# Optimization experiments

Measured on AMD Instinct MI355X. Metric: run time of the kernel, lower is better.

## Reference

```python
import jax, jax.numpy as jnp
import numpy as np

B, L, H, V = 32768, 24, 64, 64
EPS_NORM = 1e-12  # F.normalize eps
EPS_LN = 1e-5     # LayerNorm eps


def setup_inputs() -> dict:
    key = jax.random.key(0)
    ks = jax.random.split(key, 12)
    s = 1.0 / np.sqrt(H)
    init_val = float(np.log(0.9184 / (1.0 - 0.9184)))
    return {
        "seq": jax.random.randint(ks[0], (B, L), 0, V, dtype=jnp.int32),
        "embed": jax.random.normal(ks[1], (V, H), jnp.float32),
        "w1": jax.random.normal(ks[2], (H, 2 * H), jnp.float32) * s,
        "b1": jnp.zeros((2 * H,), jnp.float32),
        "w2": jax.random.normal(ks[3], (2 * H, H), jnp.float32) * s,
        "b2": jnp.zeros((H,), jnp.float32),
        "ln_g": jnp.ones((H,), jnp.float32),
        "ln_b": jnp.zeros((H,), jnp.float32),
        "rp_w": jax.random.normal(ks[4], (H, H), jnp.float32) * s,
        "rp_b": jnp.zeros((H,), jnp.float32),
        "out_w": jax.random.normal(ks[5], (H, V), jnp.float32) * s,
        "out_b": jnp.zeros((V,), jnp.float32),
        "alpha_logits": jnp.full((L,), init_val, jnp.float32),
    }


def _layernorm(x, g, b):
    mu = jnp.mean(x, axis=-1, keepdims=True)
    var = jnp.mean(jnp.square(x - mu), axis=-1, keepdims=True)
    return (x - mu) * jax.lax.rsqrt(var + EPS_LN) * g + b


def reference(seq, embed, w1, b1, w2, b2, ln_g, ln_b, rp_w, rp_b, out_w, out_b, alpha_logits):
    h = embed[seq]  # [B, L, H]
    ff = jax.nn.relu(h @ w1 + b1) @ w2 + b2
    h = _layernorm(h + ff, ln_g, ln_b)

    alphas = jax.nn.sigmoid(alpha_logits) * 0.49 + 0.5  # [L]
    ht = jnp.swapaxes(h[:, :-1, :], 0, 1)  # [L-1, B, H] time-major

    def step(M, inp):
        k, a = inp  # k: [B, H], a: scalar
        kn = k / jnp.maximum(jnp.linalg.norm(k, axis=-1, keepdims=True), EPS_NORM)
        vp = jnp.einsum('bij,bj->bi', M, kn)
        dv = k - vp
        M = M + (1.0 - a) * (dv[:, :, None] * kn[:, None, :])
        return M, None

    M0 = jnp.zeros((seq.shape[0], h.shape[-1], h.shape[-1]), h.dtype)
    M, _ = jax.lax.scan(step, M0, (ht, alphas[:-1]))

    v = jnp.einsum('bij,bj->bi', M, h[:, -1, :])
    return (v @ rp_w + rp_b) @ out_w + out_b  # [B, V]
```

## Files before the change

### kernel.cpp

```cpp
#include <hip/hip_runtime.h>
#include <hip/hip_bf16.h>
#include <math.h>

#define B_SZ 32768
#define L_SZ 24
#define H_SZ 64
#define V_SZ 64
#define ROW 68

#define HT_OFF 0
#define WK_OFF 4352
#define RN_OFF 8704
#define B2_OFF 8768
#define CF_OFF 8832
#define WS_FLOATS 8864

__global__ __launch_bounds__(128) void k_tables(
    const float* __restrict__ embed, const float* __restrict__ w1, const float* __restrict__ b1,
    const float* __restrict__ w2, const float* __restrict__ b2,
    const float* __restrict__ ln_g, const float* __restrict__ ln_b,
    float* __restrict__ ws)
{
  const int v = blockIdx.x;
  const int tid = threadIdx.x;
  __shared__ float e[H_SZ], hid[2 * H_SZ], x[H_SZ];

  if (tid < H_SZ) e[tid] = embed[v * H_SZ + tid];
  __syncthreads();

  float hj = b1[tid];
  #pragma unroll
  for (int h = 0; h < H_SZ; ++h) hj += e[h] * w1[h * (2 * H_SZ) + tid];
  hid[tid] = fmaxf(hj, 0.0f);
  __syncthreads();

  if (tid < H_SZ) {
    float f = b2[tid];
    #pragma unroll
    for (int j = 0; j < 2 * H_SZ; ++j) f += hid[j] * w2[j * H_SZ + tid];
    x[tid] = e[tid] + f;
  }
  __syncthreads();

  if (tid < H_SZ) {
    const float xi = x[tid];
    float mu = xi;
    #pragma unroll
    for (int m = 1; m < 64; m <<= 1) mu += __shfl_xor(mu, m);
    mu *= (1.0f / 64.0f);
    const float dv = xi - mu;
    float var = dv * dv;
    #pragma unroll
    for (int m = 1; m < 64; m <<= 1) var += __shfl_xor(var, m);
    var *= (1.0f / 64.0f);
    const float y = dv * rsqrtf(var + 1e-5f) * ln_g[tid] + ln_b[tid];
    ws[HT_OFF + v * ROW + tid] = y;
    float n2 = y * y;
    #pragma unroll
    for (int m = 1; m < 64; m <<= 1) n2 += __shfl_xor(n2, m);
    if (tid == 0) ws[RN_OFF + v] = 1.0f / fmaxf(sqrtf(n2), 1e-12f);
  }
}

__global__ __launch_bounds__(64) void k_proj(
    const float* __restrict__ rp_w, const float* __restrict__ rp_b,
    const float* __restrict__ out_w, const float* __restrict__ out_b,
    const float* __restrict__ alpha_logits, float* __restrict__ ws)
{
  const int i = blockIdx.x;
  const int j = threadIdx.x;
  if (i < V_SZ) {
    __shared__ float t1[H_SZ];
    float s = 0.0f;
    #pragma unroll
    for (int k = 0; k < H_SZ; ++k) s += ws[HT_OFF + i * ROW + k] * rp_w[k * H_SZ + j];
    t1[j] = s;
    __syncthreads();
    float s2 = 0.0f;
    #pragma unroll
    for (int k = 0; k < H_SZ; ++k) s2 += t1[k] * out_w[k * V_SZ + j];
    ws[WK_OFF + i * ROW + j] = s2;
  } else {
    float s = out_b[j];
    #pragma unroll
    for (int k = 0; k < H_SZ; ++k) s += rp_b[k] * out_w[k * V_SZ + j];
    ws[B2_OFF + j] = s;
    if (j < L_SZ - 1) {
      const float a = 1.0f / (1.0f + expf(-alpha_logits[j])) * 0.49f + 0.5f;
      ws[CF_OFF + j] = 1.0f - a;
    }
  }
}

__global__ __launch_bounds__(256) void k_scan(
    const int* __restrict__ seq, const float* __restrict__ ws, float* __restrict__ out)
{
  __shared__ float lds[WS_FLOATS];
  const int tid = threadIdx.x;
  for (int i = tid; i < WS_FLOATS / 4; i += 256)
    ((float4*)lds)[i] = ((const float4*)ws)[i];
  __syncthreads();

  const int lane = tid & 63;
  const int wv = tid >> 6;
  const int g = lane >> 2;
  const int s = lane & 3;
  const int batch = blockIdx.x * 64 + wv * 16 + g;
  const int s16 = s * 16;

  int sqv[L_SZ];
  const int4* sp = (const int4*)(seq + batch * L_SZ);
  #pragma unroll
  for (int i = 0; i < 6; ++i) ((int4*)sqv)[i] = sp[i];

  const float* hT = lds + HT_OFF;
  const float* wkT = lds + WK_OFF;
  const float* rnT = lds + RN_OFF;
  const float* b2T = lds + B2_OFF;
  const float* cfT = lds + CF_OFF;

  float qh[16], oa[16];
  {
    const float* qr = hT + sqv[L_SZ - 1] * ROW + s16;
    #pragma unroll
    for (int i = 0; i < 4; ++i) {
      const float4 q4 = *(const float4*)(qr + 4 * i);
      qh[4 * i + 0] = q4.x; qh[4 * i + 1] = q4.y; qh[4 * i + 2] = q4.z; qh[4 * i + 3] = q4.w;
    }
  }
  #pragma unroll
  for (int i = 0; i < 16; ++i) oa[i] = 0.0f;

  #pragma unroll
  for (int t = L_SZ - 2; t >= 0; --t) {
    const int tok = sqv[t];
    const float* kr = hT + tok * ROW + s16;
    float kv[16];
    #pragma unroll
    for (int i = 0; i < 4; ++i) {
      const float4 k4 = *(const float4*)(kr + 4 * i);
      kv[4 * i + 0] = k4.x; kv[4 * i + 1] = k4.y; kv[4 * i + 2] = k4.z; kv[4 * i + 3] = k4.w;
    }
    float p = 0.0f;
    #pragma unroll
    for (int i = 0; i < 16; ++i) p += kv[i] * qh[i];
    p += __shfl_xor(p, 1);
    p += __shfl_xor(p, 2);

    const float rnv = rnT[tok];
    const float d = p * rnv;
    const float c = cfT[t] * d;
    const float u = c * rnv;

    #pragma unroll
    for (int i = 0; i < 16; ++i) qh[i] -= u * kv[i];

    const float* wr = wkT + tok * ROW + s16;
    #pragma unroll
    for (int i = 0; i < 4; ++i) {
      const float4 w4 = *(const float4*)(wr + 4 * i);
      oa[4 * i + 0] += c * w4.x; oa[4 * i + 1] += c * w4.y;
      oa[4 * i + 2] += c * w4.z; oa[4 * i + 3] += c * w4.w;
    }
  }

  #pragma unroll
  for (int i = 0; i < 16; ++i) oa[i] += b2T[s16 + i];

  float4* op = (float4*)(out + batch * V_SZ + s16);
  #pragma unroll
  for (int i = 0; i < 4; ++i)
    op[i] = make_float4(oa[4 * i + 0], oa[4 * i + 1], oa[4 * i + 2], oa[4 * i + 3]);
}

extern "C" void kernel_launch(void* const* d_in, const int* in_sizes, int n_in,
                              void* d_out, int out_size, void* d_ws, size_t ws_size,
                              hipStream_t stream)
{
  const int*   seq          = (const int*)d_in[0];
  const float* embed        = (const float*)d_in[1];
  const float* w1           = (const float*)d_in[2];
  const float* b1           = (const float*)d_in[3];
  const float* w2           = (const float*)d_in[4];
  const float* b2           = (const float*)d_in[5];
  const float* ln_g         = (const float*)d_in[6];
  const float* ln_b         = (const float*)d_in[7];
  const float* rp_w         = (const float*)d_in[8];
  const float* rp_b         = (const float*)d_in[9];
  const float* out_w        = (const float*)d_in[10];
  const float* out_b        = (const float*)d_in[11];
  const float* alpha_logits = (const float*)d_in[12];
  float* ws  = (float*)d_ws;
  float* outp = (float*)d_out;

  hipLaunchKernelGGL(k_tables, dim3(V_SZ), dim3(128), 0, stream,
                     embed, w1, b1, w2, b2, ln_g, ln_b, ws);
  hipLaunchKernelGGL(k_proj, dim3(V_SZ + 1), dim3(64), 0, stream,
                     rp_w, rp_b, out_w, out_b, alpha_logits, ws);
  hipLaunchKernelGGL(k_scan, dim3(B_SZ / 64), dim3(256), 0, stream,
                     seq, ws, outp);
}
```

Baseline: 24.80 us.

## Fuse table kernels, pre-normalize keys, and split each batch across 8 lanes

New measurement: 29.00 us. 16.9% more time.

```diff
diff --git a/kernel.cpp b/kernel.cpp
--- a/kernel.cpp
+++ b/kernel.cpp
@@ -6,88 +6,84 @@
 #define L_SZ 24
 #define H_SZ 64
 #define V_SZ 64
-#define ROW 68
-
-#define HT_OFF 0
-#define WK_OFF 4352
-#define RN_OFF 8704
-#define B2_OFF 8768
-#define CF_OFF 8832
-#define WS_FLOATS 8864
-
-__global__ __launch_bounds__(128) void k_tables(
+
+#define KN_WS 0
+#define WK_WS 4096
+#define NRM_WS 8192
+#define B2_WS 8256
+#define CF_WS 8320
+#define WS_F 8344
+
+#define ROW 96
+#define KN_L 0
+#define WK_L 6144
+#define TL_L 12288
+#define LDS_F 12440
+
+__global__ __launch_bounds__(64) void k_tab(
     const float* __restrict__ embed, const float* __restrict__ w1, const float* __restrict__ b1,
     const float* __restrict__ w2, const float* __restrict__ b2,
     const float* __restrict__ ln_g, const float* __restrict__ ln_b,
-    float* __restrict__ ws)
-{
-  const int v = blockIdx.x;
-  const int tid = threadIdx.x;
-  __shared__ float e[H_SZ], hid[2 * H_SZ], x[H_SZ];
-
-  if (tid < H_SZ) e[tid] = embed[v * H_SZ + tid];
-  __syncthreads();
-
-  float hj = b1[tid];
-  #pragma unroll
-  for (int h = 0; h < H_SZ; ++h) hj += e[h] * w1[h * (2 * H_SZ) + tid];
-  hid[tid] = fmaxf(hj, 0.0f);
-  __syncthreads();
-
-  if (tid < H_SZ) {
-    float f = b2[tid];
-    #pragma unroll
-    for (int j = 0; j < 2 * H_SZ; ++j) f += hid[j] * w2[j * H_SZ + tid];
-    x[tid] = e[tid] + f;
-  }
-  __syncthreads();
-
-  if (tid < H_SZ) {
-    const float xi = x[tid];
-    float mu = xi;
-    #pragma unroll
-    for (int m = 1; m < 64; m <<= 1) mu += __shfl_xor(mu, m);
-    mu *= (1.0f / 64.0f);
-    const float dv = xi - mu;
-    float var = dv * dv;
-    #pragma unroll
-    for (int m = 1; m < 64; m <<= 1) var += __shfl_xor(var, m);
-    var *= (1.0f / 64.0f);
-    const float y = dv * rsqrtf(var + 1e-5f) * ln_g[tid] + ln_b[tid];
-    ws[HT_OFF + v * ROW + tid] = y;
-    float n2 = y * y;
-    #pragma unroll
-    for (int m = 1; m < 64; m <<= 1) n2 += __shfl_xor(n2, m);
-    if (tid == 0) ws[RN_OFF + v] = 1.0f / fmaxf(sqrtf(n2), 1e-12f);
-  }
-}
-
-__global__ __launch_bounds__(64) void k_proj(
     const float* __restrict__ rp_w, const float* __restrict__ rp_b,
     const float* __restrict__ out_w, const float* __restrict__ out_b,
     const float* __restrict__ alpha_logits, float* __restrict__ ws)
 {
-  const int i = blockIdx.x;
+  const int v = blockIdx.x;
   const int j = threadIdx.x;
-  if (i < V_SZ) {
-    __shared__ float t1[H_SZ];
-    float s = 0.0f;
-    #pragma unroll
-    for (int k = 0; k < H_SZ; ++k) s += ws[HT_OFF + i * ROW + k] * rp_w[k * H_SZ + j];
-    t1[j] = s;
-    __syncthreads();
-    float s2 = 0.0f;
-    #pragma unroll
-    for (int k = 0; k < H_SZ; ++k) s2 += t1[k] * out_w[k * V_SZ + j];
-    ws[WK_OFF + i * ROW + j] = s2;
+
+  if (v < V_SZ) {
+    const float ev = embed[v * H_SZ + j];
+    float h0 = b1[j], h1 = b1[j + 64];
+    #pragma unroll
+    for (int k = 0; k < H_SZ; ++k) {
+      const float ek = __shfl(ev, k);
+      h0 = fmaf(ek, w1[k * 128 + j], h0);
+      h1 = fmaf(ek, w1[k * 128 + 64 + j], h1);
+    }
+    h0 = fmaxf(h0, 0.0f);
+    h1 = fmaxf(h1, 0.0f);
+    float x = ev + b2[j];
+    #pragma unroll
+    for (int k = 0; k < H_SZ; ++k) {
+      x = fmaf(__shfl(h0, k), w2[k * H_SZ + j], x);
+      x = fmaf(__shfl(h1, k), w2[(k + 64) * H_SZ + j], x);
+    }
+    float mu = x;
+    #pragma unroll
+    for (int m = 1; m < 64; m <<= 1) mu += __shfl_xor(mu, m);
+    mu *= (1.0f / 64.0f);
+    const float dv = x - mu;
+    float var = dv * dv;
+    #pragma unroll
+    for (int m = 1; m < 64; m <<= 1) var += __shfl_xor(var, m);
+    var *= (1.0f / 64.0f);
+    const float y = dv * rsqrtf(var + 1e-5f) * ln_g[j] + ln_b[j];
+    float n2 = y * y;
+    #pragma unroll
+    for (int m = 1; m < 64; m <<= 1) n2 += __shfl_xor(n2, m);
+    const float nrm = sqrtf(n2);
+    const float rn = 1.0f / fmaxf(nrm, 1e-12f);
+    ws[KN_WS + v * H_SZ + j] = y * rn;
+    if (j == 0) ws[NRM_WS + v] = nrm;
+    float t1 = 0.0f;
+    #pragma unroll
+    for (int k = 0; k < H_SZ; ++k) t1 = fmaf(__shfl(y, k), rp_w[k * H_SZ + j], t1);
+    float wk = 0.0f;
+    #pragma unroll
+    for (int k = 0; k < H_SZ; ++k) wk = fmaf(__shfl(t1, k), out_w[k * V_SZ + j], wk);
+    ws[WK_WS + v * H_SZ + j] = wk;
   } else {
     float s = out_b[j];
     #pragma unroll
-    for (int k = 0; k < H_SZ; ++k) s += rp_b[k] * out_w[k * V_SZ + j];
-    ws[B2_OFF + j] = s;
-    if (j < L_SZ - 1) {
-      const float a = 1.0f / (1.0f + expf(-alpha_logits[j])) * 0.49f + 0.5f;
-      ws[CF_OFF + j] = 1.0f - a;
+    for (int k = 0; k < H_SZ; ++k) s = fmaf(rp_b[k], out_w[k * V_SZ + j], s);
+    ws[B2_WS + j] = s;
+    if (j < L_SZ) {
+      float cf = 0.0f;
+      if (j < L_SZ - 1) {
+        const float a = 1.0f / (1.0f + expf(-alpha_logits[j])) * 0.49f + 0.5f;
+        cf = 1.0f - a;
+      }
+      ws[CF_WS + j] = cf;
     }
   }
 }
@@ -95,82 +91,87 @@
 __global__ __launch_bounds__(256) void k_scan(
     const int* __restrict__ seq, const float* __restrict__ ws, float* __restrict__ out)
 {
-  __shared__ float lds[WS_FLOATS];
+  __shared__ float lds[LDS_F];
   const int tid = threadIdx.x;
-  for (int i = tid; i < WS_FLOATS / 4; i += 256)
-    ((float4*)lds)[i] = ((const float4*)ws)[i];
+  const float4* ws4 = (const float4*)ws;
+
+  for (int i = tid; i < 2048; i += 256) {
+    const float4 f = ws4[i];
+    float* base = (i & 1024) ? (lds + WK_L) : (lds + KN_L);
+    const int r = (i >> 4) & 63;
+    const int c = (i & 15) * 4;
+    *(float4*)(base + r * ROW + 12 * (c >> 3) + (c & 7)) = f;
+  }
+  for (int i = tid; i < 38; i += 256)
+    *(((float4*)(lds + TL_L)) + i) = ws4[2048 + i];
   __syncthreads();
+
+  const float* knL = lds + KN_L;
+  const float* wkL = lds + WK_L;
+  const float* nrmL = lds + TL_L;
+  const float* b2L = lds + TL_L + 64;
+  const float* cfL = lds + TL_L + 128;
 
   const int lane = tid & 63;
   const int wv = tid >> 6;
-  const int g = lane >> 2;
-  const int s = lane & 3;
-  const int batch = blockIdx.x * 64 + wv * 16 + g;
-  const int s16 = s * 16;
+  const int g = lane >> 3;
+  const int s = lane & 7;
+  const int batch = blockIdx.x * 32 + wv * 8 + g;
+  const int cb = 12 * s;
 
   int sqv[L_SZ];
   const int4* sp = (const int4*)(seq + batch * L_SZ);
   #pragma unroll
   for (int i = 0; i < 6; ++i) ((int4*)sqv)[i] = sp[i];
 
-  const float* hT = lds + HT_OFF;
-  const float* wkT = lds + WK_OFF;
-  const float* rnT = lds + RN_OFF;
-  const float* b2T = lds + B2_OFF;
-  const float* cfT = lds + CF_OFF;
-
-  float qh[16], oa[16];
+  float qh[8], oa[8];
   {
-    const float* qr = hT + sqv[L_SZ - 1] * ROW + s16;
-    #pragma unroll
-    for (int i = 0; i < 4; ++i) {
-      const float4 q4 = *(const float4*)(qr + 4 * i);
-      qh[4 * i + 0] = q4.x; qh[4 * i + 1] = q4.y; qh[4 * i + 2] = q4.z; qh[4 * i + 3] = q4.w;
-    }
-  }
-  #pragma unroll
-  for (int i = 0; i < 16; ++i) oa[i] = 0.0f;
+    const int tok = sqv[L_SZ - 1];
+    const float nv = nrmL[tok];
+    const float* qr = knL + tok * ROW + cb;
+    const float4 a = *(const float4*)qr;
+    const float4 b = *(const float4*)(qr + 4);
+    qh[0] = a.x * nv; qh[1] = a.y * nv; qh[2] = a.z * nv; qh[3] = a.w * nv;
+    qh[4] = b.x * nv; qh[5] = b.y * nv; qh[6] = b.z * nv; qh[7] = b.w * nv;
+  }
+  #pragma unroll
+  for (int i = 0; i < 8; ++i) oa[i] = 0.0f;
 
   #pragma unroll
   for (int t = L_SZ - 2; t >= 0; --t) {
     const int tok = sqv[t];
-    const float* kr = hT + tok * ROW + s16;
-    float kv[16];
-    #pragma unroll
-    for (int i = 0; i < 4; ++i) {
-      const float4 k4 = *(const float4*)(kr + 4 * i);
-      kv[4 * i + 0] = k4.x; kv[4 * i + 1] = k4.y; kv[4 * i + 2] = k4.z; kv[4 * i + 3] = k4.w;
-    }
+    const float* kr = knL + tok * ROW + cb;
+    const float4 ka = *(const float4*)kr;
+    const float4 kb = *(const float4*)(kr + 4);
+    float kv[8] = {ka.x, ka.y, ka.z, ka.w, kb.x, kb.y, kb.z, kb.w};
+
     float p = 0.0f;
     #pragma unroll
-    for (int i = 0; i < 16; ++i) p += kv[i] * qh[i];
+    for (int i = 0; i < 8; ++i) p = fmaf(kv[i], qh[i], p);
     p += __shfl_xor(p, 1);
     p += __shfl_xor(p, 2);
-
-    const float rnv = rnT[tok];
-    const float d = p * rnv;
-    const float c = cfT[t] * d;
-    const float u = c * rnv;
-
-    #pragma unroll
-    for (int i = 0; i < 16; ++i) qh[i] -= u * kv[i];
-
-    const float* wr = wkT + tok * ROW + s16;
-    #pragma unroll
-    for (int i = 0; i < 4; ++i) {
-      const float4 w4 = *(const float4*)(wr + 4 * i);
-      oa[4 * i + 0] += c * w4.x; oa[4 * i + 1] += c * w4.y;
-      oa[4 * i + 2] += c * w4.z; oa[4 * i + 3] += c * w4.w;
-    }
-  }
-
-  #pragma unroll
-  for (int i = 0; i < 16; ++i) oa[i] += b2T[s16 + i];
-
-  float4* op = (float4*)(out + batch * V_SZ + s16);
-  #pragma unroll
-  for (int i = 0; i < 4; ++i)
-    op[i] = make_float4(oa[4 * i + 0], oa[4 * i + 1], oa[4 * i + 2], oa[4 * i + 3]);
+    p += __shfl_xor(p, 4);
+
+    const float c = cfL[t] * p;
+
+    #pragma unroll
+    for (int i = 0; i < 8; ++i) qh[i] = fmaf(-c, kv[i], qh[i]);
+
+    const float* wr = wkL + tok * ROW + cb;
+    const float4 wa = *(const float4*)wr;
+    const float4 wb = *(const float4*)(wr + 4);
+    oa[0] = fmaf(c, wa.x, oa[0]); oa[1] = fmaf(c, wa.y, oa[1]);
+    oa[2] = fmaf(c, wa.z, oa[2]); oa[3] = fmaf(c, wa.w, oa[3]);
+    oa[4] = fmaf(c, wb.x, oa[4]); oa[5] = fmaf(c, wb.y, oa[5]);
+    oa[6] = fmaf(c, wb.z, oa[6]); oa[7] = fmaf(c, wb.w, oa[7]);
+  }
+
+  #pragma unroll
+  for (int i = 0; i < 8; ++i) oa[i] += b2L[s * 8 + i];
+
+  float4* op = (float4*)(out + batch * V_SZ + s * 8);
+  op[0] = make_float4(oa[0], oa[1], oa[2], oa[3]);
+  op[1] = make_float4(oa[4], oa[5], oa[6], oa[7]);
 }
 
 extern "C" void kernel_launch(void* const* d_in, const int* in_sizes, int n_in,
@@ -190,13 +191,12 @@
   const float* out_w        = (const float*)d_in[10];
   const float* out_b        = (const float*)d_in[11];
   const float* alpha_logits = (const float*)d_in[12];
-  float* ws  = (float*)d_ws;
+  float* ws   = (float*)d_ws;
   float* outp = (float*)d_out;
 
-  hipLaunchKernelGGL(k_tables, dim3(V_SZ), dim3(128), 0, stream,
-                     embed, w1, b1, w2, b2, ln_g, ln_b, ws);
-  hipLaunchKernelGGL(k_proj, dim3(V_SZ + 1), dim3(64), 0, stream,
+  hipLaunchKernelGGL(k_tab, dim3(V_SZ + 1), dim3(64), 0, stream,
+                     embed, w1, b1, w2, b2, ln_g, ln_b,
                      rp_w, rp_b, out_w, out_b, alpha_logits, ws);
-  hipLaunchKernelGGL(k_scan, dim3(B_SZ / 64), dim3(256), 0, stream,
+  hipLaunchKernelGGL(k_scan, dim3(B_SZ / 32), dim3(256), 0, stream,
                      seq, ws, outp);
 }
```
